# Kernel optimization log

Hardware: AMD Instinct MI355X
Metric: run time of the kernel (lower is better)

## Reference

```python
import jax, jax.numpy as jnp
import numpy as np

B, S, H, NH, K = 8, 1024, 1024, 16, 512
HD = H // NH  # head dim = 64


def setup_inputs() -> dict:
    key = jax.random.key(0)
    ks = jax.random.split(key, 9)
    hidden_states = jax.random.normal(ks[0], (B, S, H), jnp.float32)
    # remain_layers: exactly K nonzero entries per row (static max_tokens = K)
    scores = jax.random.uniform(ks[1], (B, S))
    thresh = jnp.sort(scores, axis=1)[:, S - K][:, None]
    remain_layers = (scores >= thresh).astype(jnp.int32)
    attention_mask = jnp.zeros((B, 1, 1, S), jnp.float32)  # additive mask
    init = 0.02
    Wq = jax.random.normal(ks[2], (H, H), jnp.float32) * init
    bq = jnp.zeros((H,), jnp.float32)
    Wk = jax.random.normal(ks[3], (H, H), jnp.float32) * init
    bk = jnp.zeros((H,), jnp.float32)
    Wv = jax.random.normal(ks[4], (H, H), jnp.float32) * init
    bv = jnp.zeros((H,), jnp.float32)
    return {"hidden_states": hidden_states, "attention_mask": attention_mask,
            "remain_layers": remain_layers, "Wq": Wq, "bq": bq,
            "Wk": Wk, "bk": bk, "Wv": Wv, "bv": bv}


def _heads(x):  # [B, L, H] -> [B, NH, L, HD]
    b, l, _ = x.shape
    return x.reshape(b, l, NH, HD).transpose(0, 2, 1, 3)


def reference(hidden_states, attention_mask, remain_layers, Wq, bq, Wk, bk, Wv, bv):
    # get_reduced_hidden: per-row gather of tokens with remain_layers > 0,
    # in original position order, zero-padded to max_tokens (= K here).
    order = jnp.argsort(1 - remain_layers, axis=1, stable=True)  # nonzeros first, order kept
    idx = order[:, :K]                                           # [B, K]
    reduced = jnp.take_along_axis(hidden_states, idx[:, :, None], axis=1)  # [B, K, H]
    valid = (jnp.take_along_axis(remain_layers, idx, axis=1) > 0)
    reduced = reduced * valid[:, :, None].astype(reduced.dtype)  # zero-pad slots

    q = _heads(reduced @ Wq.T + bq)          # [B, NH, K, HD]
    k = _heads(hidden_states @ Wk.T + bk)    # [B, NH, S, HD]
    v = _heads(hidden_states @ Wv.T + bv)    # [B, NH, S, HD]

    scores = jnp.einsum('bhqd,bhkd->bhqk', q, k) / np.sqrt(HD).astype(np.float32)
    scores = scores + attention_mask         # additive mask broadcast
    probs = jax.nn.softmax(scores, axis=-1)  # dropout is identity at eval
    ctx = jnp.einsum('bhqk,bhkd->bhqd', probs, v)  # [B, NH, K, HD]
    ctx = ctx.transpose(0, 2, 1, 3).reshape(B, K, H)
    return ctx
```

## Files before the change

kernel.cpp:

```cpp
#include <hip/hip_runtime.h>
#include <hip/hip_bf16.h>
#include <stdint.h>

#define S_LEN 1024
#define HDIM  1024
#define NHEADS 16
#define HEAD_D 64
#define KSEL  512
#define BATCH 8

typedef unsigned short ushort_t;
typedef __attribute__((ext_vector_type(8))) __bf16 bf16x8;
typedef __attribute__((ext_vector_type(4))) float  f32x4;

typedef const __attribute__((address_space(1))) void cg_void;
typedef __attribute__((address_space(3))) void lds_void;

__device__ __forceinline__ void gl_lds16(const void* g, void* l) {
    __builtin_amdgcn_global_load_lds((cg_void*)g, (lds_void*)l, 16, 0, 0);
}

__device__ __forceinline__ ushort_t f2bf(float f) {
    union { float f; unsigned int i; } x; x.f = f;
    unsigned int r = (x.i + 0x7fffu + ((x.i >> 16) & 1u)) >> 16;
    return (ushort_t)r;
}

__global__ __launch_bounds__(1024) void prep_kernel(
    const float* __restrict__ hidden, const float* __restrict__ wq,
    const float* __restrict__ wk, const float* __restrict__ wv,
    const int* __restrict__ remain,
    ushort_t* __restrict__ hbf, ushort_t* __restrict__ wqb,
    ushort_t* __restrict__ wkb, ushort_t* __restrict__ wvb,
    int* __restrict__ idx, int* __restrict__ valid) {
    __shared__ int wsum[16];
    __shared__ int woff[17];
    int blk = blockIdx.x;
    if (blk < 2816) {
        const float* s; ushort_t* d; int base;
        if (blk < 2048)      { s = hidden; d = hbf; base = blk; }
        else if (blk < 2304) { s = wq; d = wqb; base = blk - 2048; }
        else if (blk < 2560) { s = wk; d = wkb; base = blk - 2304; }
        else                 { s = wv; d = wvb; base = blk - 2560; }
        int i = base * 1024 + threadIdx.x;
        float4 v = ((const float4*)s)[i];
        ushort4 o;
        o.x = f2bf(v.x); o.y = f2bf(v.y); o.z = f2bf(v.z); o.w = f2bf(v.w);
        ((ushort4*)d)[i] = o;
    } else {
        int b = blk - 2816, t = threadIdx.x;
        int r = remain[b * S_LEN + t];
        unsigned long long m = __ballot(r != 0);
        int lane = t & 63, w = t >> 6;
        int pre = __popcll(m & ((1ull << lane) - 1ull));
        if (lane == 0) wsum[w] = __popcll(m);
        __syncthreads();
        if (t == 0) { int a = 0; for (int i = 0; i < 16; i++) { woff[i] = a; a += wsum[i]; } woff[16] = a; }
        __syncthreads();
        int tot = woff[16];
        int onesBefore = woff[w] + pre;
        int slot = r ? onesBefore : (tot + (t - onesBefore));
        if (slot < KSEL) { idx[b * KSEL + slot] = t; valid[b * KSEL + slot] = r; }
    }
}

#define QSCALE 0.1803368801111244f
#define LT_PITCH 136
__global__ __launch_bounds__(256, 4) void gemm_fused(
    const ushort_t* __restrict__ hbf, const ushort_t* __restrict__ wkv,
    const ushort_t* __restrict__ wq,
    const float* __restrict__ bk, const float* __restrict__ bv,
    const float* __restrict__ bq,
    const int* __restrict__ idx, const int* __restrict__ valid,
    ushort_t* __restrict__ kp, ushort_t* __restrict__ vt, ushort_t* __restrict__ qp) {
    __shared__ __align__(16) ushort_t pool[64 * LT_PITCH];
    ushort_t* As = pool;
    ushort_t* Bs = pool + 4096;
    const int i = blockIdx.x;
    int z, bmI, bnI;
    if (i < 1024) { z = 0; int x = i & 7, j = i >> 3; bmI = x * 8 + (j >> 4); bnI = j & 15; }
    else          { z = 1; int q = i - 1024;          bmI = q >> 3;           bnI = q & 7;  }
    const long bm = (long)bmI * 128;
    const int bn = bnI * 128;

    const int tid = threadIdx.x;
    const int lane = tid & 63;
    const int w = tid >> 6;
    const int quad = lane >> 4;
    const int cl = lane & 15;
    const int srow = w * 16 + (lane >> 2);
    const int scol = (lane & 3) * 8;
    const int lds_off = w * 512 + lane * 8;
    const int wr = (w >> 1) * 64, wc = (w & 1) * 64;

    const ushort_t* W = z ? wq : wkv;

    long ab[2];
#pragma unroll
    for (int p = 0; p < 2; p++) {
        long gr = bm + p * 64 + srow;
        if (z == 0) ab[p] = gr * HDIM;
        else {
            int b_ = (int)(gr >> 9);
            int src = idx[(b_ << 9) + ((int)gr & 511)];
            ab[p] = ((long)(b_ << 10) + src) * HDIM;
        }
    }

    f32x4 acc[4][4] = {};

    for (int k0 = 0; k0 < HDIM; k0 += 32) {
#pragma unroll
        for (int p = 0; p < 2; p++) {
            gl_lds16(hbf + ab[p] + k0 + scol, &As[p * 2048 + lds_off]);
            gl_lds16(W + ((long)(bn + p * 64 + srow)) * HDIM + k0 + scol, &Bs[p * 2048 + lds_off]);
        }
        __syncthreads();
        bf16x8 af[4], bfr[4];
#pragma unroll
        for (int mt = 0; mt < 4; mt++)
            af[mt] = *(const bf16x8*)&As[(wr + mt * 16 + cl) * 32 + quad * 8];
#pragma unroll
        for (int nt = 0; nt < 4; nt++)
            bfr[nt] = *(const bf16x8*)&Bs[(wc + nt * 16 + cl) * 32 + quad * 8];
#pragma unroll
        for (int mt = 0; mt < 4; mt++)
#pragma unroll
            for (int nt = 0; nt < 4; nt++)
                acc[mt][nt] = __builtin_amdgcn_mfma_f32_16x16x32_bf16(af[mt], bfr[nt], acc[mt][nt], 0, 0, 0);
        __syncthreads();
    }

    if (z == 1) {
#pragma unroll
        for (int nt = 0; nt < 4; nt++) {
            int col = bn + wc + nt * 16 + cl;
            float bvq = bq[col];
#pragma unroll
            for (int mt = 0; mt < 4; mt++) {
                long row = bm + wr + mt * 16 + quad * 4;
#pragma unroll
                for (int r = 0; r < 4; r++) {
                    float vm = (float)valid[row + r];
                    qp[(row + r) * HDIM + col] = f2bf((acc[mt][nt][r] * vm + bvq) * QSCALE);
                }
            }
        }
    } else if (bn < 1024) {
#pragma unroll
        for (int nt = 0; nt < 4; nt++) {
            int col = bn + wc + nt * 16 + cl;
            float bvk = bk[col];
#pragma unroll
            for (int mt = 0; mt < 4; mt++) {
                long row = bm + wr + mt * 16 + quad * 4;
#pragma unroll
                for (int r = 0; r < 4; r++)
                    kp[(row + r) * HDIM + col] = f2bf(acc[mt][nt][r] + bvk);
            }
        }
    } else {
        ushort_t* Lt = pool;
        long b_ = bm >> 10, s0 = bm & 1023;
#pragma unroll
        for (int p2 = 0; p2 < 2; p2++) {
            if ((w & 1) == p2) {
#pragma unroll
                for (int nt = 0; nt < 4; nt++) {
                    int cloc = nt * 16 + cl;
                    float bvv = bv[bn - 1024 + p2 * 64 + cloc];
#pragma unroll
                    for (int mt = 0; mt < 4; mt++) {
                        int row0 = wr + mt * 16 + quad * 4;
#pragma unroll
                        for (int r = 0; r < 4; r++)
                            Lt[cloc * LT_PITCH + row0 + r] = f2bf(acc[mt][nt][r] + bvv);
                    }
                }
            }
            __syncthreads();
            int c2 = tid >> 2, quarter = tid & 3;
            long gbase = ((b_ << 10) + (bn - 1024) + p2 * 64 + c2) * 1024 + s0 + quarter * 32;
            const ushort_t* src = Lt + c2 * LT_PITCH + quarter * 32;
#pragma unroll
            for (int q8 = 0; q8 < 4; q8++)
                *(bf16x8*)(vt + gbase + q8 * 8) = *(const bf16x8*)(src + q8 * 8);
            __syncthreads();
        }
    }
}

#define P_PITCH 72
__global__ __launch_bounds__(512, 4) void attn_kernel(
    const ushort_t* __restrict__ qp, const ushort_t* __restrict__ kp,
    const ushort_t* __restrict__ vt, const float* __restrict__ mask,
    float* __restrict__ out) {
    __shared__ __align__(16) ushort_t ks[2][2 * 64 * 32];
    __shared__ __align__(16) ushort_t vs[2][2 * 64 * 32];
    __shared__ __align__(16) ushort_t ps[8][16 * P_PITCH];
    const int tid = threadIdx.x;
    const int lane = tid & 63;
    const int w = tid >> 6;
    const int quad = lane >> 4;
    const int cl = lane & 15;
    const int qt = blockIdx.x, h = blockIdx.y, b = blockIdx.z;

    const int skk = tid >> 8;
    const int ss  = (tid & 255) >> 2;
    const int sc8 = (tid & 3) * 8;
    const int lds_off = tid * 8;

    const long kbase = (long)b * S_LEN;
    const long vbase = (long)b * 1024 + h * HEAD_D;

    const long qrow = (long)b * KSEL + qt * 128 + w * 16 + cl;
    bf16x8 aq[2];
#pragma unroll
    for (int kk = 0; kk < 2; kk++)
        aq[kk] = *(const bf16x8*)(qp + qrow * HDIM + h * HEAD_D + kk * 32 + quad * 8);

    f32x4 O[4] = {};
    float l_r[4] = {0.f, 0.f, 0.f, 0.f};

    gl_lds16(kp + (kbase + ss) * (long)HDIM + h * HEAD_D + skk * 32 + sc8, &ks[0][lds_off]);
    gl_lds16(vt + (vbase + ss) * (long)S_LEN + skk * 32 + sc8, &vs[0][lds_off]);

    for (int c = 0; c < S_LEN / 64; c++) {
        __asm__ volatile("s_waitcnt vmcnt(0)" ::: "memory");
        __syncthreads();
        if (c + 1 < S_LEN / 64) {
            int nb = (c + 1) & 1;
            gl_lds16(kp + (kbase + (c + 1) * 64 + ss) * (long)HDIM + h * HEAD_D + skk * 32 + sc8,
                     &ks[nb][lds_off]);
            gl_lds16(vt + (vbase + ss) * (long)S_LEN + (c + 1) * 64 + skk * 32 + sc8,
                     &vs[nb][lds_off]);
        }
        const ushort_t* kbuf = ks[c & 1];
        const ushort_t* vbuf = vs[c & 1];

        f32x4 sc[4] = {};
#pragma unroll
        for (int kk = 0; kk < 2; kk++) {
#pragma unroll
            for (int nt = 0; nt < 4; nt++) {
                bf16x8 bk8 = *(const bf16x8*)&kbuf[kk * 2048 + (nt * 16 + cl) * 32 + quad * 8];
                sc[nt] = __builtin_amdgcn_mfma_f32_16x16x32_bf16(aq[kk], bk8, sc[nt], 0, 0, 0);
            }
        }
#pragma unroll
        for (int nt = 0; nt < 4; nt++) {
            float mv = mask[b * S_LEN + c * 64 + nt * 16 + cl] * 1.44269504f;
#pragma unroll
            for (int r = 0; r < 4; r++) {
                float p_ = __builtin_amdgcn_exp2f(sc[nt][r] + mv);
                sc[nt][r] = p_;
                l_r[r] += p_;
            }
        }

#pragma unroll
        for (int nt = 0; nt < 4; nt++)
#pragma unroll
            for (int r = 0; r < 4; r++)
                ps[w][(quad * 4 + r) * P_PITCH + nt * 16 + cl] = f2bf(sc[nt][r]);

        __asm__ volatile("s_waitcnt lgkmcnt(0)" ::: "memory");

#pragma unroll
        for (int kk = 0; kk < 2; kk++) {
            bf16x8 ap = *(const bf16x8*)&ps[w][cl * P_PITCH + kk * 32 + quad * 8];
#pragma unroll
            for (int dt = 0; dt < 4; dt++) {
                bf16x8 bv8 = *(const bf16x8*)&vbuf[kk * 2048 + (dt * 16 + cl) * 32 + quad * 8];
                O[dt] = __builtin_amdgcn_mfma_f32_16x16x32_bf16(ap, bv8, O[dt], 0, 0, 0);
            }
        }
    }

#pragma unroll
    for (int r = 0; r < 4; r++) {
        float s0 = l_r[r];
#pragma unroll
        for (int d = 1; d < 16; d <<= 1) s0 += __shfl_xor(s0, d, 64);
        l_r[r] = s0;
    }

    const long orow0 = (long)b * KSEL + qt * 128 + w * 16 + quad * 4;
#pragma unroll
    for (int dt = 0; dt < 4; dt++) {
        int col = h * HEAD_D + dt * 16 + cl;
#pragma unroll
        for (int r = 0; r < 4; r++)
            out[(orow0 + r) * HDIM + col] = O[dt][r] / l_r[r];
    }
}

extern "C" void kernel_launch(void* const* d_in, const int* in_sizes, int n_in,
                              void* d_out, int out_size, void* d_ws, size_t ws_size,
                              hipStream_t stream) {
    const float* hidden = (const float*)d_in[0];
    const float* mask   = (const float*)d_in[1];
    const int*   remain = (const int*)d_in[2];
    const float* Wq = (const float*)d_in[3];
    const float* bq = (const float*)d_in[4];
    const float* Wk = (const float*)d_in[5];
    const float* bk = (const float*)d_in[6];
    const float* Wv = (const float*)d_in[7];
    const float* bv = (const float*)d_in[8];
    float* out = (float*)d_out;

    char* ws = (char*)d_ws;
    size_t off = 0;
    int* idx   = (int*)(ws + off); off += 16384;
    int* valid = (int*)(ws + off); off += 16384;
    ushort_t* hbf = (ushort_t*)(ws + off); off += (size_t)BATCH * S_LEN * HDIM * 2;
    ushort_t* wqb = (ushort_t*)(ws + off); off += (size_t)HDIM * HDIM * 2;
    ushort_t* wkb = (ushort_t*)(ws + off); off += (size_t)HDIM * HDIM * 2;
    ushort_t* wvb = (ushort_t*)(ws + off); off += (size_t)HDIM * HDIM * 2;
    ushort_t* qp  = (ushort_t*)(ws + off); off += (size_t)BATCH * KSEL * HDIM * 2;
    ushort_t* kp  = (ushort_t*)(ws + off); off += (size_t)BATCH * S_LEN * HDIM * 2;
    ushort_t* vt  = (ushort_t*)(ws + off); off += (size_t)BATCH * S_LEN * HDIM * 2;

    prep_kernel<<<2824, 1024, 0, stream>>>(hidden, Wq, Wk, Wv, remain,
                                           hbf, wqb, wkb, wvb, idx, valid);
    gemm_fused<<<1280, 256, 0, stream>>>(hbf, wkb, wqb, bk, bv, bq,
                                         idx, valid, kp, vt, qp);
    attn_kernel<<<dim3(4, NHEADS, BATCH), 512, 0, stream>>>(qp, kp, vt, mask, out);
}
```

Baseline: 204.4 us.

## Deepen GEMM K-tile to 64 and give attention waves 32 query rows

The QKV GEMM now stages two 32-wide K slices per iteration, which halves the number of barrier pairs at the cost of twice the LDS. The attention kernel switches from 8 waves of 16 query rows to 4 waves of 32 rows. Each K and V fragment read from LDS is reused across two MFMA row tiles, and loads are split across fewer threads. This trades fewer waves per block, and so less latency hiding, for more register-level reuse.

```diff
diff --git a/kernel.cpp b/kernel.cpp
--- a/kernel.cpp
+++ b/kernel.cpp
@@ -73,9 +73,9 @@
     const float* __restrict__ bq,
     const int* __restrict__ idx, const int* __restrict__ valid,
     ushort_t* __restrict__ kp, ushort_t* __restrict__ vt, ushort_t* __restrict__ qp) {
-    __shared__ __align__(16) ushort_t pool[64 * LT_PITCH];
+    __shared__ __align__(16) ushort_t pool[16384];
     ushort_t* As = pool;
-    ushort_t* Bs = pool + 4096;
+    ushort_t* Bs = pool + 8192;
     const int i = blockIdx.x;
     int z, bmI, bnI;
     if (i < 1024) { z = 0; int x = i & 7, j = i >> 3; bmI = x * 8 + (j >> 4); bnI = j & 15; }
@@ -109,25 +109,31 @@
 
     f32x4 acc[4][4] = {};
 
-    for (int k0 = 0; k0 < HDIM; k0 += 32) {
-#pragma unroll
-        for (int p = 0; p < 2; p++) {
-            gl_lds16(hbf + ab[p] + k0 + scol, &As[p * 2048 + lds_off]);
-            gl_lds16(W + ((long)(bn + p * 64 + srow)) * HDIM + k0 + scol, &Bs[p * 2048 + lds_off]);
-        }
-        __syncthreads();
-        bf16x8 af[4], bfr[4];
-#pragma unroll
-        for (int mt = 0; mt < 4; mt++)
-            af[mt] = *(const bf16x8*)&As[(wr + mt * 16 + cl) * 32 + quad * 8];
-#pragma unroll
-        for (int nt = 0; nt < 4; nt++)
-            bfr[nt] = *(const bf16x8*)&Bs[(wc + nt * 16 + cl) * 32 + quad * 8];
-#pragma unroll
-        for (int mt = 0; mt < 4; mt++)
+    for (int k0 = 0; k0 < HDIM; k0 += 64) {
+#pragma unroll
+        for (int p = 0; p < 2; p++)
+#pragma unroll
+            for (int hh = 0; hh < 2; hh++) {
+                gl_lds16(hbf + ab[p] + k0 + hh * 32 + scol, &As[hh * 4096 + p * 2048 + lds_off]);
+                gl_lds16(W + ((long)(bn + p * 64 + srow)) * HDIM + k0 + hh * 32 + scol,
+                         &Bs[hh * 4096 + p * 2048 + lds_off]);
+            }
+        __syncthreads();
+#pragma unroll
+        for (int hh = 0; hh < 2; hh++) {
+            bf16x8 af[4], bfr[4];
+#pragma unroll
+            for (int mt = 0; mt < 4; mt++)
+                af[mt] = *(const bf16x8*)&As[hh * 4096 + (wr + mt * 16 + cl) * 32 + quad * 8];
 #pragma unroll
             for (int nt = 0; nt < 4; nt++)
-                acc[mt][nt] = __builtin_amdgcn_mfma_f32_16x16x32_bf16(af[mt], bfr[nt], acc[mt][nt], 0, 0, 0);
+                bfr[nt] = *(const bf16x8*)&Bs[hh * 4096 + (wc + nt * 16 + cl) * 32 + quad * 8];
+#pragma unroll
+            for (int mt = 0; mt < 4; mt++)
+#pragma unroll
+                for (int nt = 0; nt < 4; nt++)
+                    acc[mt][nt] = __builtin_amdgcn_mfma_f32_16x16x32_bf16(af[mt], bfr[nt], acc[mt][nt], 0, 0, 0);
+        }
         __syncthreads();
     }
 
@@ -191,13 +197,13 @@
 }
 
 #define P_PITCH 72
-__global__ __launch_bounds__(512, 4) void attn_kernel(
+__global__ __launch_bounds__(256, 2) void attn_kernel(
     const ushort_t* __restrict__ qp, const ushort_t* __restrict__ kp,
     const ushort_t* __restrict__ vt, const float* __restrict__ mask,
     float* __restrict__ out) {
-    __shared__ __align__(16) ushort_t ks[2][2 * 64 * 32];
-    __shared__ __align__(16) ushort_t vs[2][2 * 64 * 32];
-    __shared__ __align__(16) ushort_t ps[8][16 * P_PITCH];
+    __shared__ __align__(16) ushort_t ks[2][4096];
+    __shared__ __align__(16) ushort_t vs[2][4096];
+    __shared__ __align__(16) ushort_t ps[4][32 * P_PITCH];
     const int tid = threadIdx.x;
     const int lane = tid & 63;
     const int w = tid >> 6;
@@ -205,93 +211,116 @@
     const int cl = lane & 15;
     const int qt = blockIdx.x, h = blockIdx.y, b = blockIdx.z;
 
-    const int skk = tid >> 8;
-    const int ss  = (tid & 255) >> 2;
+    const int srow = tid >> 2;
     const int sc8 = (tid & 3) * 8;
     const int lds_off = tid * 8;
 
     const long kbase = (long)b * S_LEN;
     const long vbase = (long)b * 1024 + h * HEAD_D;
 
-    const long qrow = (long)b * KSEL + qt * 128 + w * 16 + cl;
-    bf16x8 aq[2];
-#pragma unroll
-    for (int kk = 0; kk < 2; kk++)
-        aq[kk] = *(const bf16x8*)(qp + qrow * HDIM + h * HEAD_D + kk * 32 + quad * 8);
-
-    f32x4 O[4] = {};
-    float l_r[4] = {0.f, 0.f, 0.f, 0.f};
-
-    gl_lds16(kp + (kbase + ss) * (long)HDIM + h * HEAD_D + skk * 32 + sc8, &ks[0][lds_off]);
-    gl_lds16(vt + (vbase + ss) * (long)S_LEN + skk * 32 + sc8, &vs[0][lds_off]);
+    const long qrow0 = (long)b * KSEL + qt * 128 + w * 32;
+    bf16x8 aq[2][2];
+#pragma unroll
+    for (int mt = 0; mt < 2; mt++)
+#pragma unroll
+        for (int kk = 0; kk < 2; kk++)
+            aq[mt][kk] = *(const bf16x8*)(qp + (qrow0 + mt * 16 + cl) * HDIM + h * HEAD_D + kk * 32 + quad * 8);
+
+    f32x4 O[2][4] = {};
+    float l_r[2][4] = {};
+
+#pragma unroll
+    for (int j = 0; j < 2; j++) {
+        gl_lds16(kp + (kbase + srow) * (long)HDIM + h * HEAD_D + j * 32 + sc8, &ks[0][j * 2048 + lds_off]);
+        gl_lds16(vt + (vbase + srow) * (long)S_LEN + j * 32 + sc8, &vs[0][j * 2048 + lds_off]);
+    }
 
     for (int c = 0; c < S_LEN / 64; c++) {
         __asm__ volatile("s_waitcnt vmcnt(0)" ::: "memory");
         __syncthreads();
         if (c + 1 < S_LEN / 64) {
             int nb = (c + 1) & 1;
-            gl_lds16(kp + (kbase + (c + 1) * 64 + ss) * (long)HDIM + h * HEAD_D + skk * 32 + sc8,
-                     &ks[nb][lds_off]);
-            gl_lds16(vt + (vbase + ss) * (long)S_LEN + (c + 1) * 64 + skk * 32 + sc8,
-                     &vs[nb][lds_off]);
+#pragma unroll
+            for (int j = 0; j < 2; j++) {
+                gl_lds16(kp + (kbase + (c + 1) * 64 + srow) * (long)HDIM + h * HEAD_D + j * 32 + sc8,
+                         &ks[nb][j * 2048 + lds_off]);
+                gl_lds16(vt + (vbase + srow) * (long)S_LEN + (c + 1) * 64 + j * 32 + sc8,
+                         &vs[nb][j * 2048 + lds_off]);
+            }
         }
         const ushort_t* kbuf = ks[c & 1];
         const ushort_t* vbuf = vs[c & 1];
 
-        f32x4 sc[4] = {};
-#pragma unroll
-        for (int kk = 0; kk < 2; kk++) {
+        f32x4 sc[2][4] = {};
+#pragma unroll
+        for (int kk = 0; kk < 2; kk++)
 #pragma unroll
             for (int nt = 0; nt < 4; nt++) {
                 bf16x8 bk8 = *(const bf16x8*)&kbuf[kk * 2048 + (nt * 16 + cl) * 32 + quad * 8];
-                sc[nt] = __builtin_amdgcn_mfma_f32_16x16x32_bf16(aq[kk], bk8, sc[nt], 0, 0, 0);
-            }
-        }
+#pragma unroll
+                for (int mt = 0; mt < 2; mt++)
+                    sc[mt][nt] = __builtin_amdgcn_mfma_f32_16x16x32_bf16(aq[mt][kk], bk8, sc[mt][nt], 0, 0, 0);
+            }
+
 #pragma unroll
         for (int nt = 0; nt < 4; nt++) {
             float mv = mask[b * S_LEN + c * 64 + nt * 16 + cl] * 1.44269504f;
 #pragma unroll
-            for (int r = 0; r < 4; r++) {
-                float p_ = __builtin_amdgcn_exp2f(sc[nt][r] + mv);
-                sc[nt][r] = p_;
-                l_r[r] += p_;
-            }
-        }
-
-#pragma unroll
-        for (int nt = 0; nt < 4; nt++)
-#pragma unroll
-            for (int r = 0; r < 4; r++)
-                ps[w][(quad * 4 + r) * P_PITCH + nt * 16 + cl] = f2bf(sc[nt][r]);
+            for (int mt = 0; mt < 2; mt++)
+#pragma unroll
+                for (int r = 0; r < 4; r++) {
+                    float p_ = __builtin_amdgcn_exp2f(sc[mt][nt][r] + mv);
+                    sc[mt][nt][r] = p_;
+                    l_r[mt][r] += p_;
+                }
+        }
+
+#pragma unroll
+        for (int mt = 0; mt < 2; mt++)
+#pragma unroll
+            for (int nt = 0; nt < 4; nt++)
+#pragma unroll
+                for (int r = 0; r < 4; r++)
+                    ps[w][(mt * 16 + quad * 4 + r) * P_PITCH + nt * 16 + cl] = f2bf(sc[mt][nt][r]);
 
         __asm__ volatile("s_waitcnt lgkmcnt(0)" ::: "memory");
 
 #pragma unroll
         for (int kk = 0; kk < 2; kk++) {
-            bf16x8 ap = *(const bf16x8*)&ps[w][cl * P_PITCH + kk * 32 + quad * 8];
+            bf16x8 ap[2];
+#pragma unroll
+            for (int mt = 0; mt < 2; mt++)
+                ap[mt] = *(const bf16x8*)&ps[w][(mt * 16 + cl) * P_PITCH + kk * 32 + quad * 8];
 #pragma unroll
             for (int dt = 0; dt < 4; dt++) {
                 bf16x8 bv8 = *(const bf16x8*)&vbuf[kk * 2048 + (dt * 16 + cl) * 32 + quad * 8];
-                O[dt] = __builtin_amdgcn_mfma_f32_16x16x32_bf16(ap, bv8, O[dt], 0, 0, 0);
-            }
-        }
-    }
-
-#pragma unroll
-    for (int r = 0; r < 4; r++) {
-        float s0 = l_r[r];
-#pragma unroll
-        for (int d = 1; d < 16; d <<= 1) s0 += __shfl_xor(s0, d, 64);
-        l_r[r] = s0;
-    }
-
-    const long orow0 = (long)b * KSEL + qt * 128 + w * 16 + quad * 4;
-#pragma unroll
-    for (int dt = 0; dt < 4; dt++) {
-        int col = h * HEAD_D + dt * 16 + cl;
-#pragma unroll
-        for (int r = 0; r < 4; r++)
-            out[(orow0 + r) * HDIM + col] = O[dt][r] / l_r[r];
+#pragma unroll
+                for (int mt = 0; mt < 2; mt++)
+                    O[mt][dt] = __builtin_amdgcn_mfma_f32_16x16x32_bf16(ap[mt], bv8, O[mt][dt], 0, 0, 0);
+            }
+        }
+    }
+
+#pragma unroll
+    for (int mt = 0; mt < 2; mt++)
+#pragma unroll
+        for (int r = 0; r < 4; r++) {
+            float s0 = l_r[mt][r];
+#pragma unroll
+            for (int d = 1; d < 16; d <<= 1) s0 += __shfl_xor(s0, d, 64);
+            l_r[mt][r] = s0;
+        }
+
+#pragma unroll
+    for (int mt = 0; mt < 2; mt++) {
+        const long orow0 = qrow0 + mt * 16 + quad * 4;
+#pragma unroll
+        for (int dt = 0; dt < 4; dt++) {
+            int col = h * HEAD_D + dt * 16 + cl;
+#pragma unroll
+            for (int r = 0; r < 4; r++)
+                out[(orow0 + r) * HDIM + col] = O[mt][dt][r] / l_r[mt][r];
+        }
     }
 }
 
@@ -325,5 +354,5 @@
                                            hbf, wqb, wkb, wvb, idx, valid);
     gemm_fused<<<1280, 256, 0, stream>>>(hbf, wkb, wqb, bk, bv, bq,
                                          idx, valid, kp, vt, qp);
-    attn_kernel<<<dim3(4, NHEADS, BATCH), 512, 0, stream>>>(qp, kp, vt, mask, out);
-}
+    attn_kernel<<<dim3(4, NHEADS, BATCH), 256, 0, stream>>>(qp, kp, vt, mask, out);
+}
```

After: 199.2 us. -2.6%, faster.
